# Kernel optimization log

Hardware: AMD Instinct MI355X
Metric: run time of the kernel (lower is better)

The kernel has to match this reference:

```python
import jax, jax.numpy as jnp
import numpy as np

N = 50000          # residues
E = 1000000        # edges
H = 128            # hidden_channels
CUT = 11.5         # cutoff
NR = 6             # num_radial
NS = 3             # num_spherical
NPE = 16           # num_pos_emb

def swish(x):
    return x * jax.nn.sigmoid(x)

def rbf(d):
    # Bessel-style radial basis with smooth cosine cutoff, [E, NR]
    u = jnp.clip(d / CUT, 0.0, 1.0)
    n = jnp.arange(1, NR + 1, dtype=jnp.float32)
    fc = 0.5 * (jnp.cos(jnp.pi * u) + 1.0)
    return jnp.sqrt(2.0 / CUT) * jnp.sin(n * jnp.pi * u[:, None]) / (d[:, None] + 1e-6) * fc[:, None]

def angle_emb(d, ang):
    # d_angle_emb: radial x cos(l*angle) -> [E, NR*NS]
    r = rbf(d)
    l = jnp.arange(NS, dtype=jnp.float32)
    a = jnp.cos(ang[:, None] * l)
    return (r[:, :, None] * a[:, None, :]).reshape(d.shape[0], NR * NS)

def theta_phi_emb(d, theta, phi):
    # d_theta_phi_emb: radial x angular(theta) x angular(phi) -> [E, NR*NS*NS]
    r = rbf(d)
    l = jnp.arange(NS, dtype=jnp.float32)
    ct = jnp.cos(theta[:, None] * l)
    cp = jnp.cos(phi[:, None] * l)
    return jnp.einsum('en,el,em->enlm', r, ct, cp).reshape(d.shape[0], NR * NS * NS)


def setup_inputs():
    key = jax.random.key(0)
    ks = jax.random.split(key, 20)
    f32 = jnp.float32
    pos = jax.random.normal(ks[0], (N, 3), f32) * 8.0
    pos_n = pos + jax.random.normal(ks[1], (N, 3), f32) * 0.8
    pos_c = pos + jax.random.normal(ks[2], (N, 3), f32) * 0.8
    z = jax.random.randint(ks[3], (N,), 0, 26)
    bb_embs = jax.random.normal(ks[4], (N, 6), f32)
    side_chain_embs = jax.random.normal(ks[5], (N, 8), f32)
    esm_embs = jax.random.normal(ks[6], (N, 1280), f32)
    batch = jnp.zeros((N,), jnp.int32)
    edge_index = jax.random.randint(ks[7], (2, E), 0, N)
    def w(k, shape):
        return jax.random.normal(k, shape, f32) * (1.0 / np.sqrt(shape[0]))
    edge_in = NR * NS * NS + 3 * NR * NS + NPE  # 54 + 54 + 16 = 124
    params = dict(
        W_emb=w(ks[8], (26 + 6 + 8, H // 2)), b_emb=jnp.zeros((H // 2,), f32),
        W_esm=w(ks[9], (1280, H // 2)), b_esm=jnp.zeros((H // 2,), f32),
        W_edge=w(ks[10], (edge_in, H)),
        W_msg=w(ks[11], (H, H)),
        W_upd=w(ks[12], (H, H)),
        W_o0=w(ks[13], (H, H)), b_o0=jnp.zeros((H,), f32),
        W_o1=w(ks[14], (H, 32)), b_o1=jnp.zeros((32,), f32),
        W_of=w(ks[15], (32, 1)), b_of=jnp.zeros((1,), f32),
        W_n0=w(ks[16], (H, 32)), b_n0=jnp.zeros((32,), f32),
        W_nf=w(ks[17], (32, 2)), b_nf=jnp.zeros((2,), f32),
    )
    return dict(z=z, pos=pos, pos_n=pos_n, pos_c=pos_c, bb_embs=bb_embs,
                side_chain_embs=side_chain_embs, esm_embs=esm_embs,
                batch=batch, edge_index=edge_index, **params)


def reference(z, pos, pos_n, pos_c, bb_embs, side_chain_embs, esm_embs, batch,
              edge_index, W_emb, b_emb, W_esm, b_esm, W_edge, W_msg, W_upd,
              W_o0, b_o0, W_o1, b_o1, W_of, b_of, W_n0, b_n0, W_nf, b_nf):
    # --- node embedding fusion (level='allatom+esm') ---
    oh = jax.nn.one_hot(z, 26, dtype=jnp.float32)
    x_a = jnp.concatenate([oh, bb_embs, side_chain_embs], axis=1) @ W_emb + b_emb
    x_s = esm_embs @ W_esm + b_esm
    x = jnp.concatenate([x_a, x_s], axis=-1)  # [N, H]

    j, i = edge_index[0], edge_index[1]

    # --- sinusoidal positional embedding of sequence offsets ---
    dpe = (j - i).astype(jnp.float32)
    freq = jnp.exp(jnp.arange(0, NPE, 2, dtype=jnp.float32) * (-np.log(10000.0) / NPE))
    ang = dpe[:, None] * freq
    pe = jnp.concatenate([jnp.cos(ang), jnp.sin(ang)], axis=-1)  # [E, NPE]

    # --- distance / theta / phi (triplet gathers via sequence neighbors) ---
    v_ji = pos[j] - pos[i]
    dist = jnp.linalg.norm(pos[i] - pos[j], axis=1)
    refi0 = (i - 1) % N
    refi1 = (i + 1) % N
    v_r0 = pos[refi0] - pos[i]
    v_r1 = pos[refi1] - pos[i]
    a = jnp.sum(v_ji * v_r0, axis=-1)
    b = jnp.linalg.norm(jnp.cross(v_ji, v_r0), axis=-1)
    theta = jnp.arctan2(b, a)
    p1 = jnp.cross(v_r0, v_r1)
    p2 = jnp.cross(v_r0, v_ji)
    a = jnp.sum(p1 * p2, axis=-1)
    b = jnp.sum(jnp.cross(p1, p2) * v_r0, axis=-1) / (jnp.linalg.norm(v_r0, axis=-1) + 1e-7)
    phi = jnp.arctan2(b, a)
    feature0 = theta_phi_emb(dist, theta, phi)  # [E, 54]

    # --- backbone-frame Euler angles (allatom branch) ---
    o1x = pos_n[i] - pos[i]
    o1z = jnp.cross(o1x, jnp.cross(o1x, pos_c[i] - pos[i]))
    o1zl = jnp.linalg.norm(o1z, axis=1) + 1e-7
    o2x = pos_n[j] - pos[j]
    o2z = jnp.cross(o2x, jnp.cross(o2x, pos_c[j] - pos[j]))
    o2zl = jnp.linalg.norm(o2z, axis=1) + 1e-7
    nvec = jnp.cross(o1z, o2z)
    angle1 = jnp.arctan2(jnp.sum(jnp.cross(o1x, nvec) * o1z, -1) / o1zl, jnp.sum(o1x * nvec, -1))
    angle2 = jnp.arctan2(jnp.linalg.norm(nvec, axis=-1), jnp.sum(o1z * o2z, -1))
    angle3 = jnp.arctan2(jnp.sum(jnp.cross(nvec, o2x) * o2z, -1) / o2zl, jnp.sum(nvec * o2x, -1))
    feature1 = jnp.concatenate([angle_emb(dist, angle1), angle_emb(dist, angle2),
                                angle_emb(dist, angle3)], axis=1)  # [E, 54]

    # --- message passing (gather-compute-scatter stand-in for model_E) ---
    ef = swish(jnp.concatenate([feature0, feature1, pe], axis=-1) @ W_edge)  # [E, H]
    m = swish(x[j] @ W_msg) * ef
    agg = jax.ops.segment_sum(m, i, num_segments=N)
    xe = x + swish(agg @ W_upd)

    # --- output heads (dropout inactive at inference) ---
    xn = jax.nn.relu(x @ W_n0 + b_n0)
    node_out = xn @ W_nf + b_nf                   # [N, 2]
    h = jax.nn.relu(xe @ W_o0 + b_o0)
    h = jax.nn.relu(h @ W_o1 + b_o1)
    out = jax.nn.sigmoid(h @ W_of + b_of)         # [N, 1]
    return out, node_out
```

## Files before the change

kernel.cpp:

```cpp
#include <hip/hip_runtime.h>
#include <math.h>
#include <stdint.h>

#define NRES 50000
#define NEDGE 1000000
#define PI_F 3.14159265358979323846f

typedef __attribute__((ext_vector_type(8))) short short8;
typedef __attribute__((ext_vector_type(4))) float floatx4;
typedef __attribute__((ext_vector_type(2))) short bf16x2;
typedef __attribute__((address_space(1))) bf16x2* gbf16x2p;

struct f3 { float x, y, z; };
__device__ __forceinline__ f3 ld3(const float* __restrict__ p, int i) {
  return {p[3*i+0], p[3*i+1], p[3*i+2]};
}
__device__ __forceinline__ f3 f3sub(f3 a, f3 b){ return {a.x-b.x, a.y-b.y, a.z-b.z}; }
__device__ __forceinline__ f3 f3cross(f3 a, f3 b){
  return {a.y*b.z - a.z*b.y, a.z*b.x - a.x*b.z, a.x*b.y - a.y*b.x};
}
__device__ __forceinline__ float f3dot(f3 a, f3 b){ return a.x*b.x + a.y*b.y + a.z*b.z; }
__device__ __forceinline__ float swish_fast(float v){
  return v * __builtin_amdgcn_rcpf(1.0f + __expf(-v));
}
__device__ __forceinline__ short f2bf(float f){
  unsigned u = __float_as_uint(f);
  unsigned r = (u + 0x7fffu + ((u >> 16) & 1u)) >> 16;
  return (short)r;
}
__device__ __forceinline__ float bf2f(short s){
  return __uint_as_float(((unsigned)(unsigned short)s) << 16);
}
__device__ __forceinline__ float cos_atan2(float y, float x){
  return x * __builtin_amdgcn_rsqf(fmaxf(x*x + y*y, 1e-30f));
}
__device__ __forceinline__ void atom_pk_bf16(short* addr, bf16x2 v){
  __builtin_amdgcn_global_atomic_fadd_v2bf16((gbf16x2p)(uintptr_t)addr, v);
}

__global__ __launch_bounds__(256) void k_wprep(
    const float* __restrict__ We, const float* __restrict__ Wm,
    const float* __restrict__ Ws, const float* __restrict__ Wu,
    const float* __restrict__ Wo0, const float* __restrict__ Wn0,
    const float* __restrict__ Wo1,
    short* __restrict__ Wef, short* __restrict__ Wmf, short* __restrict__ Wsf,
    short* __restrict__ Wuf, short* __restrict__ Wo0f,
    short* __restrict__ Wn0f, short* __restrict__ Wo1f)
{
  int gid = blockIdx.x * 256 + threadIdx.x;
  const float* src; short* dst; int NT, K, N, t;
  if      (gid < 16384)  { t = gid;          src = We;  dst = Wef;  NT = 8; K = 124;  N = 128; }
  else if (gid < 32768)  { t = gid - 16384;  src = Wm;  dst = Wmf;  NT = 8; K = 128;  N = 128; }
  else if (gid < 114688) { t = gid - 32768;  src = Ws;  dst = Wsf;  NT = 4; K = 1280; N = 64;  }
  else if (gid < 131072) { t = gid - 114688; src = Wu;  dst = Wuf;  NT = 8; K = 128;  N = 128; }
  else if (gid < 147456) { t = gid - 131072; src = Wo0; dst = Wo0f; NT = 8; K = 128;  N = 128; }
  else if (gid < 151552) { t = gid - 147456; src = Wn0; dst = Wn0f; NT = 2; K = 128;  N = 32;  }
  else if (gid < 155648) { t = gid - 151552; src = Wo1; dst = Wo1f; NT = 2; K = 128;  N = 32;  }
  else return;
  int j = t & 7, lane = (t >> 3) & 63;
  int rest = t >> 9;
  int nt = rest % NT, kt = rest / NT;
  int k = kt*32 + (lane >> 4)*8 + j, n = nt*16 + (lane & 15);
  dst[t] = f2bf((k < K) ? src[k*N + n] : 0.0f);
}

__global__ __launch_bounds__(256) void k_xa(
    const int* __restrict__ z, const float* __restrict__ bb,
    const float* __restrict__ side, const float* __restrict__ W_emb,
    const float* __restrict__ b_emb, short* __restrict__ xb)
{
  int tid = threadIdx.x;
  int h = tid & 63;
  int n = blockIdx.x * 4 + (tid >> 6);
  if (n >= NRES) return;
  int zz = z[n];
  float acc = W_emb[zz * 64 + h] + b_emb[h];
  #pragma unroll
  for (int k = 0; k < 6; ++k) acc += bb[n*6 + k] * W_emb[(26 + k)*64 + h];
  #pragma unroll
  for (int k = 0; k < 8; ++k) acc += side[n*8 + k] * W_emb[(32 + k)*64 + h];
  xb[(size_t)n * 128 + h] = f2bf(acc);
}

__global__ __launch_bounds__(256) void k_esm(
    const float* __restrict__ esm, const short* __restrict__ Wsf,
    const float* __restrict__ b, short* __restrict__ xb)
{
  const int tid = threadIdx.x;
  const int lane = tid & 63, w = tid >> 6;
  const int quad = lane >> 4, colb = lane & 15;
  const int tile0 = blockIdx.x * 64 + w * 16;

  int arow = tile0 + colb;
  if (arow >= NRES) arow = NRES - 1;
  const float* ap = esm + (size_t)arow * 1280 + quad * 8;

  floatx4 acc[4];
  #pragma unroll
  for (int nt = 0; nt < 4; ++nt) acc[nt] = (floatx4){0.f, 0.f, 0.f, 0.f};

  for (int kt = 0; kt < 40; ++kt) {
    float4 v0 = *(const float4*)(ap + kt*32);
    float4 v1 = *(const float4*)(ap + kt*32 + 4);
    short8 a;
    a[0] = f2bf(v0.x); a[1] = f2bf(v0.y); a[2] = f2bf(v0.z); a[3] = f2bf(v0.w);
    a[4] = f2bf(v1.x); a[5] = f2bf(v1.y); a[6] = f2bf(v1.z); a[7] = f2bf(v1.w);
    #pragma unroll
    for (int nt = 0; nt < 4; ++nt) {
      short8 bf = *(const short8*)&Wsf[(size_t)((kt*4 + nt)*64 + lane)*8];
      acc[nt] = __builtin_amdgcn_mfma_f32_16x16x32_bf16(a, bf, acc[nt], 0, 0, 0);
    }
  }
  #pragma unroll
  for (int nt = 0; nt < 4; ++nt) {
    int ch = nt*16 + colb;
    float bias = b[ch];
    #pragma unroll
    for (int r = 0; r < 4; ++r) {
      int n = tile0 + quad*4 + r;
      if (n < NRES) xb[(size_t)n * 128 + 64 + ch] = f2bf(acc[nt][r] + bias);
    }
  }
}

__global__ __launch_bounds__(256, 4) void k_edge(
    const int* __restrict__ ei, const float* __restrict__ pos,
    const float* __restrict__ posn, const float* __restrict__ posc,
    const short* __restrict__ xb, const short* __restrict__ Wef,
    const short* __restrict__ Wmf, short* __restrict__ aggb)
{
  __shared__ int sJ[64];
  __shared__ int sI[64];
  __shared__ __align__(16) short sF[64][136];
  __shared__ __align__(16) short sXJ[64][136];

  const int tid = threadIdx.x;
  const int e0 = blockIdx.x * 64;

  if (tid < 64) { sJ[tid] = ei[e0 + tid]; sI[tid] = ei[NEDGE + e0 + tid]; }
  __syncthreads();

  if (tid < 64) {
    const int e = tid;
    const int j = sJ[e], i = sI[e];
    f3 pj = ld3(pos, j), pi = ld3(pos, i);
    f3 vji = f3sub(pj, pi);
    float nji2 = f3dot(vji, vji);
    float dist = sqrtf(nji2);
    int r0i = (i == 0) ? (NRES - 1) : (i - 1);
    int r1i = (i == NRES - 1) ? 0 : (i + 1);
    f3 vr0 = f3sub(ld3(pos, r0i), pi);
    f3 vr1 = f3sub(ld3(pos, r1i), pi);
    float nr02 = f3dot(vr0, vr0);

    float ct = f3dot(vji, vr0) * __builtin_amdgcn_rsqf(fmaxf(nji2 * nr02, 1e-30f));
    f3 p1 = f3cross(vr0, vr1);
    f3 p2 = f3cross(vr0, vji);
    float pa = f3dot(p1, p2);
    float pb = f3dot(f3cross(p1, p2), vr0) / (sqrtf(nr02) + 1e-7f);
    float cp = cos_atan2(pb, pa);

    f3 pni = ld3(posn, i), pci = ld3(posc, i);
    f3 o1x = f3sub(pni, pi);
    f3 o1z = f3cross(o1x, f3cross(o1x, f3sub(pci, pi)));
    float no1z2 = f3dot(o1z, o1z);
    float o1zl = sqrtf(no1z2) + 1e-7f;
    f3 pnj = ld3(posn, j), pcj = ld3(posc, j);
    f3 o2x = f3sub(pnj, pj);
    f3 o2z = f3cross(o2x, f3cross(o2x, f3sub(pcj, pj)));
    float no2z2 = f3dot(o2z, o2z);
    float o2zl = sqrtf(no2z2) + 1e-7f;
    f3 nv = f3cross(o1z, o2z);
    float y1 = f3dot(f3cross(o1x, nv), o1z) / o1zl;
    float ca1 = cos_atan2(y1, f3dot(o1x, nv));
    float ca2 = f3dot(o1z, o2z) * __builtin_amdgcn_rsqf(fmaxf(no1z2 * no2z2, 1e-30f));
    float y3 = f3dot(f3cross(nv, o2x), o2z) / o2zl;
    float ca3 = cos_atan2(y3, f3dot(nv, o2x));

    float u = fminf(dist * (1.0f/11.5f), 1.0f);
    float spu, cpu;
    __sincosf(PI_F * u, &spu, &cpu);
    float fc = 0.5f * (cpu + 1.0f);
    float pref = 0.41702882811414954f * __builtin_amdgcn_rcpf(dist + 1e-6f) * fc;
    float rb[6];
    {
      float twoc = 2.0f * cpu;
      float s_nm1 = 0.0f, s_n = spu;
      #pragma unroll
      for (int nn = 0; nn < 6; ++nn) {
        rb[nn] = pref * s_n;
        float s_np1 = twoc * s_n - s_nm1;
        s_nm1 = s_n; s_n = s_np1;
      }
    }

    float ctv[3] = {1.0f, ct, 2.0f*ct*ct - 1.0f};
    float cpv[3] = {1.0f, cp, 2.0f*cp*cp - 1.0f};
    #pragma unroll
    for (int nn = 0; nn < 6; ++nn)
      #pragma unroll
      for (int l = 0; l < 3; ++l)
        #pragma unroll
        for (int m = 0; m < 3; ++m)
          sF[e][nn*9 + l*3 + m] = f2bf(rb[nn] * ctv[l] * cpv[m]);

    float cas[3] = {ca1, ca2, ca3};
    #pragma unroll
    for (int t = 0; t < 3; ++t) {
      float c = cas[t];
      float cav[3] = {1.0f, c, 2.0f*c*c - 1.0f};
      #pragma unroll
      for (int nn = 0; nn < 6; ++nn)
        #pragma unroll
        for (int l = 0; l < 3; ++l)
          sF[e][54 + t*18 + nn*3 + l] = f2bf(rb[nn] * cav[l]);
    }

    const float FRQ[8] = {1.0f, 0.31622776601683794f, 0.1f, 0.03162277660168379f,
                          0.01f, 0.003162277660168379f, 0.001f, 0.0003162277660168379f};
    float dpe = (float)(j - i);
    #pragma unroll
    for (int q = 0; q < 8; ++q) {
      float s, c;
      __sincosf(dpe * FRQ[q], &s, &c);
      sF[e][108 + q] = f2bf(c);
      sF[e][116 + q] = f2bf(s);
    }
    sF[e][124] = 0; sF[e][125] = 0; sF[e][126] = 0; sF[e][127] = 0;
  } else {
    const int t2 = tid - 64;
    for (int it = 0; it < 6; ++it) {
      int idx = it * 192 + t2;
      if (idx < 1024) {
        int row = idx >> 4;
        int c8 = idx & 15;
        *(short8*)&sXJ[row][c8*8] = *(const short8*)&xb[(size_t)sJ[row] * 128 + c8*8];
      }
    }
  }
  __syncthreads();

  const int lane = tid & 63, w = tid >> 6;
  const int quad = lane >> 4, colb = lane & 15;
  const int nb = w * 2;

  short8 bE[4][2], bM[4][2];
  #pragma unroll
  for (int kt = 0; kt < 4; ++kt)
    #pragma unroll
    for (int nt = 0; nt < 2; ++nt) {
      bE[kt][nt] = *(const short8*)&Wef[(size_t)((kt*8 + nb + nt)*64 + lane)*8];
      bM[kt][nt] = *(const short8*)&Wmf[(size_t)((kt*8 + nb + nt)*64 + lane)*8];
    }

  floatx4 accE[4][2], accM[4][2];
  #pragma unroll
  for (int mt = 0; mt < 4; ++mt)
    #pragma unroll
    for (int nt = 0; nt < 2; ++nt) {
      accE[mt][nt] = (floatx4){0.f, 0.f, 0.f, 0.f};
      accM[mt][nt] = (floatx4){0.f, 0.f, 0.f, 0.f};
    }

  #pragma unroll
  for (int kt = 0; kt < 4; ++kt) {
    #pragma unroll
    for (int mt = 0; mt < 4; ++mt) {
      short8 af = *(const short8*)&sF [mt*16 + colb][kt*32 + quad*8];
      short8 ax = *(const short8*)&sXJ[mt*16 + colb][kt*32 + quad*8];
      #pragma unroll
      for (int nt = 0; nt < 2; ++nt) {
        accE[mt][nt] = __builtin_amdgcn_mfma_f32_16x16x32_bf16(af, bE[kt][nt], accE[mt][nt], 0, 0, 0);
        accM[mt][nt] = __builtin_amdgcn_mfma_f32_16x16x32_bf16(ax, bM[kt][nt], accM[mt][nt], 0, 0, 0);
      }
    }
  }
  __syncthreads();

  short (*sM)[136] = sXJ;
  #pragma unroll
  for (int mt = 0; mt < 4; ++mt)
    #pragma unroll
    for (int nt = 0; nt < 2; ++nt) {
      int ch = w*32 + nt*16 + colb;
      #pragma unroll
      for (int r = 0; r < 4; ++r) {
        int e = mt*16 + quad*4 + r;
        sM[e][ch] = f2bf(swish_fast(accM[mt][nt][r]) * swish_fast(accE[mt][nt][r]));
      }
    }
  __syncthreads();

  #pragma unroll
  for (int it = 0; it < 16; ++it) {
    int flat = it * 256 + tid;
    int row = flat >> 6, p = flat & 63;
    bf16x2 v = *(const bf16x2*)&sM[row][p*2];
    atom_pk_bf16(&aggb[(size_t)sI[row] * 128 + p*2], v);
  }
}

__global__ __launch_bounds__(256) void k_upd(
    const short* __restrict__ xb, const short* __restrict__ aggb,
    const short* __restrict__ Wuf, const short* __restrict__ Wo0f,
    const short* __restrict__ Wn0f, const short* __restrict__ Wo1f,
    const float* __restrict__ bn0, const float* __restrict__ Wnf,
    const float* __restrict__ bnf, const float* __restrict__ bo0,
    const float* __restrict__ bo1, const float* __restrict__ Wof,
    const float* __restrict__ bof, float* __restrict__ out0,
    float* __restrict__ out1)
{
  __shared__ __align__(16) short sA[64][136];
  __shared__ __align__(16) short sX[64][136];
  __shared__ float sS[64][33];

  const int tid = threadIdx.x;
  const int lane = tid & 63, w = tid >> 6;
  const int quad = lane >> 4, colb = lane & 15;
  const int n0 = blockIdx.x * 64;

  #pragma unroll
  for (int it = 0; it < 4; ++it) {
    int idx = it * 256 + tid;
    int row = idx >> 4, c8 = idx & 15;
    int n = n0 + row;
    short8 va = (short8)(short)0, vx = (short8)(short)0;
    if (n < NRES) {
      va = *(const short8*)&aggb[(size_t)n * 128 + c8*8];
      vx = *(const short8*)&xb  [(size_t)n * 128 + c8*8];
    }
    *(short8*)&sA[row][c8*8] = va;
    *(short8*)&sX[row][c8*8] = vx;
  }
  __syncthreads();

  {
    floatx4 accN[2];
    accN[0] = (floatx4){0.f,0.f,0.f,0.f}; accN[1] = (floatx4){0.f,0.f,0.f,0.f};
    #pragma unroll
    for (int kt = 0; kt < 4; ++kt) {
      short8 a = *(const short8*)&sX[w*16 + colb][kt*32 + quad*8];
      #pragma unroll
      for (int nt = 0; nt < 2; ++nt) {
        short8 bf = *(const short8*)&Wn0f[(size_t)((kt*2 + nt)*64 + lane)*8];
        accN[nt] = __builtin_amdgcn_mfma_f32_16x16x32_bf16(a, bf, accN[nt], 0, 0, 0);
      }
    }
    #pragma unroll
    for (int nt = 0; nt < 2; ++nt) {
      int col = nt*16 + colb;
      float bias = bn0[col];
      #pragma unroll
      for (int r = 0; r < 4; ++r)
        sS[w*16 + quad*4 + r][col] = fmaxf(accN[nt][r] + bias, 0.0f);
    }
  }
  __syncthreads();
  if (tid < 128) {
    int row = tid >> 1, oc = tid & 1;
    int n = n0 + row;
    if (n < NRES) {
      float a2 = bnf[oc];
      #pragma unroll
      for (int k = 0; k < 32; ++k) a2 += sS[row][k] * Wnf[k*2 + oc];
      out1[(size_t)n * 2 + oc] = a2;
    }
  }

  floatx4 acc1[4][2];
  #pragma unroll
  for (int mt = 0; mt < 4; ++mt) {
    acc1[mt][0] = (floatx4){0.f,0.f,0.f,0.f};
    acc1[mt][1] = (floatx4){0.f,0.f,0.f,0.f};
  }
  #pragma unroll
  for (int kt = 0; kt < 4; ++kt) {
    short8 b0 = *(const short8*)&Wuf[(size_t)((kt*8 + w*2 + 0)*64 + lane)*8];
    short8 b1 = *(const short8*)&Wuf[(size_t)((kt*8 + w*2 + 1)*64 + lane)*8];
    #pragma unroll
    for (int mt = 0; mt < 4; ++mt) {
      short8 a = *(const short8*)&sA[mt*16 + colb][kt*32 + quad*8];
      acc1[mt][0] = __builtin_amdgcn_mfma_f32_16x16x32_bf16(a, b0, acc1[mt][0], 0, 0, 0);
      acc1[mt][1] = __builtin_amdgcn_mfma_f32_16x16x32_bf16(a, b1, acc1[mt][1], 0, 0, 0);
    }
  }
  __syncthreads();
  #pragma unroll
  for (int mt = 0; mt < 4; ++mt)
    #pragma unroll
    for (int nt = 0; nt < 2; ++nt)
      #pragma unroll
      for (int r = 0; r < 4; ++r) {
        int row = mt*16 + quad*4 + r, col = w*32 + nt*16 + colb;
        float xv = bf2f(sX[row][col]);
        sA[row][col] = f2bf(xv + swish_fast(acc1[mt][nt][r]));
      }
  __syncthreads();

  floatx4 acc2[4][2];
  #pragma unroll
  for (int mt = 0; mt < 4; ++mt) {
    acc2[mt][0] = (floatx4){0.f,0.f,0.f,0.f};
    acc2[mt][1] = (floatx4){0.f,0.f,0.f,0.f};
  }
  #pragma unroll
  for (int kt = 0; kt < 4; ++kt) {
    short8 b0 = *(const short8*)&Wo0f[(size_t)((kt*8 + w*2 + 0)*64 + lane)*8];
    short8 b1 = *(const short8*)&Wo0f[(size_t)((kt*8 + w*2 + 1)*64 + lane)*8];
    #pragma unroll
    for (int mt = 0; mt < 4; ++mt) {
      short8 a = *(const short8*)&sA[mt*16 + colb][kt*32 + quad*8];
      acc2[mt][0] = __builtin_amdgcn_mfma_f32_16x16x32_bf16(a, b0, acc2[mt][0], 0, 0, 0);
      acc2[mt][1] = __builtin_amdgcn_mfma_f32_16x16x32_bf16(a, b1, acc2[mt][1], 0, 0, 0);
    }
  }
  __syncthreads();
  #pragma unroll
  for (int mt = 0; mt < 4; ++mt)
    #pragma unroll
    for (int nt = 0; nt < 2; ++nt) {
      int col = w*32 + nt*16 + colb;
      float bias = bo0[col];
      #pragma unroll
      for (int r = 0; r < 4; ++r) {
        int row = mt*16 + quad*4 + r;
        sX[row][col] = f2bf(fmaxf(acc2[mt][nt][r] + bias, 0.0f));
      }
    }
  __syncthreads();

  {
    floatx4 accH[2];
    accH[0] = (floatx4){0.f,0.f,0.f,0.f}; accH[1] = (floatx4){0.f,0.f,0.f,0.f};
    #pragma unroll
    for (int kt = 0; kt < 4; ++kt) {
      short8 a = *(const short8*)&sX[w*16 + colb][kt*32 + quad*8];
      #pragma unroll
      for (int nt = 0; nt < 2; ++nt) {
        short8 bf = *(const short8*)&Wo1f[(size_t)((kt*2 + nt)*64 + lane)*8];
        accH[nt] = __builtin_amdgcn_mfma_f32_16x16x32_bf16(a, bf, accH[nt], 0, 0, 0);
      }
    }
    __syncthreads();
    #pragma unroll
    for (int nt = 0; nt < 2; ++nt) {
      int col = nt*16 + colb;
      float bias = bo1[col];
      #pragma unroll
      for (int r = 0; r < 4; ++r)
        sS[w*16 + quad*4 + r][col] = fmaxf(accH[nt][r] + bias, 0.0f);
    }
  }
  __syncthreads();

  if (tid < 64) {
    int n = n0 + tid;
    if (n < NRES) {
      float a2 = bof[0];
      #pragma unroll
      for (int k = 0; k < 32; ++k) a2 += sS[tid][k] * Wof[k];
      out0[n] = 1.0f / (1.0f + expf(-a2));
    }
  }
}

extern "C" void kernel_launch(void* const* d_in, const int* in_sizes, int n_in,
                              void* d_out, int out_size, void* d_ws, size_t ws_size,
                              hipStream_t stream) {
  (void)in_sizes; (void)n_in; (void)out_size; (void)ws_size;
  const int*   z     = (const int*)  d_in[0];
  const float* pos   = (const float*)d_in[1];
  const float* posn  = (const float*)d_in[2];
  const float* posc  = (const float*)d_in[3];
  const float* bb    = (const float*)d_in[4];
  const float* side  = (const float*)d_in[5];
  const float* esm   = (const float*)d_in[6];
  const int*   ei    = (const int*)  d_in[8];
  const float* W_emb = (const float*)d_in[9];
  const float* b_emb = (const float*)d_in[10];
  const float* W_esm = (const float*)d_in[11];
  const float* b_esm = (const float*)d_in[12];
  const float* W_edge= (const float*)d_in[13];
  const float* W_msg = (const float*)d_in[14];
  const float* W_upd = (const float*)d_in[15];
  const float* W_o0  = (const float*)d_in[16];
  const float* b_o0  = (const float*)d_in[17];
  const float* W_o1  = (const float*)d_in[18];
  const float* b_o1  = (const float*)d_in[19];
  const float* W_of  = (const float*)d_in[20];
  const float* b_of  = (const float*)d_in[21];
  const float* W_n0  = (const float*)d_in[22];
  const float* b_n0  = (const float*)d_in[23];
  const float* W_nf  = (const float*)d_in[24];
  const float* b_nf  = (const float*)d_in[25];

  char* ws = (char*)d_ws;
  short* xb   = (short*)ws;
  short* aggb = (short*)(ws + 12800000);
  short* Wef  = (short*)(ws + 25600000);
  short* Wmf  = (short*)(ws + 25632768);
  short* Wsf  = (short*)(ws + 25665536);
  short* Wuf  = (short*)(ws + 25829376);
  short* Wo0f = (short*)(ws + 25862144);
  short* Wn0f = (short*)(ws + 25894912);
  short* Wo1f = (short*)(ws + 25903104);
  float* out0 = (float*)d_out;
  float* out1 = out0 + NRES;

  hipMemsetAsync(aggb, 0, (size_t)NRES * 128 * sizeof(short), stream);

  k_wprep<<<608, 256, 0, stream>>>(W_edge, W_msg, W_esm, W_upd, W_o0, W_n0, W_o1,
                                   Wef, Wmf, Wsf, Wuf, Wo0f, Wn0f, Wo1f);
  k_xa   <<<12500, 256, 0, stream>>>(z, bb, side, W_emb, b_emb, xb);
  k_esm  <<<782,   256, 0, stream>>>(esm, Wsf, b_esm, xb);
  k_edge <<<15625, 256, 0, stream>>>(ei, pos, posn, posc, xb, Wef, Wmf, aggb);
  k_upd  <<<782,   256, 0, stream>>>(xb, aggb, Wuf, Wo0f, Wn0f, Wo1f,
                                     b_n0, W_nf, b_nf, b_o0, b_o1, W_of, b_of,
                                     out0, out1);
}
```

Baseline: 712.0 us.

## Precompute per-node message transform and sort edges by destination for segmented atomics

Moves the swish(x[j] @ W_msg) projection out of the per-edge kernel into a per-node k_msg kernel, so the edge kernel gathers precomputed messages instead of doing a second GEMM for every edge. Edges are counting-sorted by destination (histogram, scan, scatter) into a permutation, and the edge kernel walks sorted edges, reducing rows with the same destination locally before issuing bf16 atomics. Blocks are remapped across XCDs so contiguous sorted chunks stay together. This adds several small sort kernels and a permuted gather, and it runs only when the workspace is large enough, otherwise falling back to the old path.

```diff
diff --git a/kernel.cpp b/kernel.cpp
--- a/kernel.cpp
+++ b/kernel.cpp
@@ -5,6 +5,7 @@
 #define NRES 50000
 #define NEDGE 1000000
 #define PI_F 3.14159265358979323846f
+#define NSEG 196
 
 typedef __attribute__((ext_vector_type(8))) short short8;
 typedef __attribute__((ext_vector_type(4))) float floatx4;
@@ -36,6 +37,97 @@
 }
 __device__ __forceinline__ void atom_pk_bf16(short* addr, bf16x2 v){
   __builtin_amdgcn_global_atomic_fadd_v2bf16((gbf16x2p)(uintptr_t)addr, v);
+}
+
+__device__ __forceinline__ void edge_features(
+    int e, int j, int i,
+    const float* __restrict__ pos, const float* __restrict__ posn,
+    const float* __restrict__ posc, short (*sF)[136])
+{
+  f3 pj = ld3(pos, j), pi = ld3(pos, i);
+  f3 vji = f3sub(pj, pi);
+  float nji2 = f3dot(vji, vji);
+  float dist = sqrtf(nji2);
+  int r0i = (i == 0) ? (NRES - 1) : (i - 1);
+  int r1i = (i == NRES - 1) ? 0 : (i + 1);
+  f3 vr0 = f3sub(ld3(pos, r0i), pi);
+  f3 vr1 = f3sub(ld3(pos, r1i), pi);
+  float nr02 = f3dot(vr0, vr0);
+
+  float ct = f3dot(vji, vr0) * __builtin_amdgcn_rsqf(fmaxf(nji2 * nr02, 1e-30f));
+  f3 p1 = f3cross(vr0, vr1);
+  f3 p2 = f3cross(vr0, vji);
+  float pa = f3dot(p1, p2);
+  float pb = f3dot(f3cross(p1, p2), vr0) / (sqrtf(nr02) + 1e-7f);
+  float cp = cos_atan2(pb, pa);
+
+  f3 pni = ld3(posn, i), pci = ld3(posc, i);
+  f3 o1x = f3sub(pni, pi);
+  f3 o1z = f3cross(o1x, f3cross(o1x, f3sub(pci, pi)));
+  float no1z2 = f3dot(o1z, o1z);
+  float o1zl = sqrtf(no1z2) + 1e-7f;
+  f3 pnj = ld3(posn, j), pcj = ld3(posc, j);
+  f3 o2x = f3sub(pnj, pj);
+  f3 o2z = f3cross(o2x, f3cross(o2x, f3sub(pcj, pj)));
+  float no2z2 = f3dot(o2z, o2z);
+  float o2zl = sqrtf(no2z2) + 1e-7f;
+  f3 nv = f3cross(o1z, o2z);
+  float y1 = f3dot(f3cross(o1x, nv), o1z) / o1zl;
+  float ca1 = cos_atan2(y1, f3dot(o1x, nv));
+  float ca2 = f3dot(o1z, o2z) * __builtin_amdgcn_rsqf(fmaxf(no1z2 * no2z2, 1e-30f));
+  float y3 = f3dot(f3cross(nv, o2x), o2z) / o2zl;
+  float ca3 = cos_atan2(y3, f3dot(nv, o2x));
+
+  float u = fminf(dist * (1.0f/11.5f), 1.0f);
+  float spu, cpu;
+  __sincosf(PI_F * u, &spu, &cpu);
+  float fc = 0.5f * (cpu + 1.0f);
+  float pref = 0.41702882811414954f * __builtin_amdgcn_rcpf(dist + 1e-6f) * fc;
+  float rb[6];
+  {
+    float twoc = 2.0f * cpu;
+    float s_nm1 = 0.0f, s_n = spu;
+    #pragma unroll
+    for (int nn = 0; nn < 6; ++nn) {
+      rb[nn] = pref * s_n;
+      float s_np1 = twoc * s_n - s_nm1;
+      s_nm1 = s_n; s_n = s_np1;
+    }
+  }
+
+  float ctv[3] = {1.0f, ct, 2.0f*ct*ct - 1.0f};
+  float cpv[3] = {1.0f, cp, 2.0f*cp*cp - 1.0f};
+  #pragma unroll
+  for (int nn = 0; nn < 6; ++nn)
+    #pragma unroll
+    for (int l = 0; l < 3; ++l)
+      #pragma unroll
+      for (int m = 0; m < 3; ++m)
+        sF[e][nn*9 + l*3 + m] = f2bf(rb[nn] * ctv[l] * cpv[m]);
+
+  float cas[3] = {ca1, ca2, ca3};
+  #pragma unroll
+  for (int t = 0; t < 3; ++t) {
+    float c = cas[t];
+    float cav[3] = {1.0f, c, 2.0f*c*c - 1.0f};
+    #pragma unroll
+    for (int nn = 0; nn < 6; ++nn)
+      #pragma unroll
+      for (int l = 0; l < 3; ++l)
+        sF[e][54 + t*18 + nn*3 + l] = f2bf(rb[nn] * cav[l]);
+  }
+
+  const float FRQ[8] = {1.0f, 0.31622776601683794f, 0.1f, 0.03162277660168379f,
+                        0.01f, 0.003162277660168379f, 0.001f, 0.0003162277660168379f};
+  float dpe = (float)(j - i);
+  #pragma unroll
+  for (int q = 0; q < 8; ++q) {
+    float s, c;
+    __sincosf(dpe * FRQ[q], &s, &c);
+    sF[e][108 + q] = f2bf(c);
+    sF[e][116 + q] = f2bf(s);
+  }
+  sF[e][124] = 0; sF[e][125] = 0; sF[e][126] = 0; sF[e][127] = 0;
 }
 
 __global__ __launch_bounds__(256) void k_wprep(
@@ -64,6 +156,68 @@
   dst[t] = f2bf((k < K) ? src[k*N + n] : 0.0f);
 }
 
+__global__ __launch_bounds__(256) void k_hist(
+    const int* __restrict__ ei, int* __restrict__ bins)
+{
+  int e = blockIdx.x * 256 + threadIdx.x;
+  if (e < NEDGE) atomicAdd(&bins[ei[NEDGE + e]], 1);
+}
+
+__global__ __launch_bounds__(256) void k_scan1(
+    int* __restrict__ bins, int* __restrict__ bsum)
+{
+  __shared__ int s[256];
+  const int t = threadIdx.x, b = blockIdx.x;
+  const int idx = b * 256 + t;
+  int v = (idx < NRES) ? bins[idx] : 0;
+  s[t] = v;
+  __syncthreads();
+  #pragma unroll
+  for (int d = 1; d < 256; d <<= 1) {
+    int add = (t >= d) ? s[t - d] : 0;
+    __syncthreads();
+    if (t >= d) s[t] += add;
+    __syncthreads();
+  }
+  if (idx < NRES) bins[idx] = s[t] - v;
+  if (t == 255) bsum[b] = s[255];
+}
+
+__global__ __launch_bounds__(256) void k_scan2(int* __restrict__ bsum)
+{
+  __shared__ int s[256];
+  const int t = threadIdx.x;
+  int v = (t < NSEG) ? bsum[t] : 0;
+  s[t] = v;
+  __syncthreads();
+  #pragma unroll
+  for (int d = 1; d < 256; d <<= 1) {
+    int add = (t >= d) ? s[t - d] : 0;
+    __syncthreads();
+    if (t >= d) s[t] += add;
+    __syncthreads();
+  }
+  if (t < NSEG) bsum[t] = s[t] - v;
+}
+
+__global__ __launch_bounds__(256) void k_scan3(
+    int* __restrict__ bins, const int* __restrict__ bsum)
+{
+  int idx = blockIdx.x * 256 + threadIdx.x;
+  if (idx < NRES) bins[idx] += bsum[blockIdx.x];
+}
+
+__global__ __launch_bounds__(256) void k_scatter(
+    const int* __restrict__ ei, int* __restrict__ bins, int* __restrict__ perm)
+{
+  int e = blockIdx.x * 256 + threadIdx.x;
+  if (e < NEDGE) {
+    int i = ei[NEDGE + e];
+    int slot = atomicAdd(&bins[i], 1);
+    if (slot >= 0 && slot < NEDGE) perm[slot] = e;
+  }
+}
+
 __global__ __launch_bounds__(256) void k_xa(
     const int* __restrict__ z, const float* __restrict__ bb,
     const float* __restrict__ side, const float* __restrict__ W_emb,
@@ -123,7 +277,172 @@
   }
 }
 
-__global__ __launch_bounds__(256, 4) void k_edge(
+__global__ __launch_bounds__(256) void k_msg(
+    const short* __restrict__ xb, const short* __restrict__ Wmf,
+    short* __restrict__ xmb)
+{
+  __shared__ __align__(16) short sX[64][136];
+  __shared__ __align__(16) short sO[64][136];
+  const int tid = threadIdx.x;
+  const int lane = tid & 63, w = tid >> 6;
+  const int quad = lane >> 4, colb = lane & 15;
+  const int n0 = blockIdx.x * 64;
+
+  #pragma unroll
+  for (int it = 0; it < 4; ++it) {
+    int idx = it * 256 + tid;
+    int row = idx >> 4, c8 = idx & 15;
+    int n = n0 + row;
+    short8 v = (short8)(short)0;
+    if (n < NRES) v = *(const short8*)&xb[(size_t)n * 128 + c8*8];
+    *(short8*)&sX[row][c8*8] = v;
+  }
+  __syncthreads();
+
+  floatx4 acc[4][2];
+  #pragma unroll
+  for (int mt = 0; mt < 4; ++mt) {
+    acc[mt][0] = (floatx4){0.f,0.f,0.f,0.f};
+    acc[mt][1] = (floatx4){0.f,0.f,0.f,0.f};
+  }
+  #pragma unroll
+  for (int kt = 0; kt < 4; ++kt) {
+    short8 b0 = *(const short8*)&Wmf[(size_t)((kt*8 + w*2 + 0)*64 + lane)*8];
+    short8 b1 = *(const short8*)&Wmf[(size_t)((kt*8 + w*2 + 1)*64 + lane)*8];
+    #pragma unroll
+    for (int mt = 0; mt < 4; ++mt) {
+      short8 a = *(const short8*)&sX[mt*16 + colb][kt*32 + quad*8];
+      acc[mt][0] = __builtin_amdgcn_mfma_f32_16x16x32_bf16(a, b0, acc[mt][0], 0, 0, 0);
+      acc[mt][1] = __builtin_amdgcn_mfma_f32_16x16x32_bf16(a, b1, acc[mt][1], 0, 0, 0);
+    }
+  }
+  #pragma unroll
+  for (int mt = 0; mt < 4; ++mt)
+    #pragma unroll
+    for (int nt = 0; nt < 2; ++nt)
+      #pragma unroll
+      for (int r = 0; r < 4; ++r)
+        sO[mt*16 + quad*4 + r][w*32 + nt*16 + colb] = f2bf(swish_fast(acc[mt][nt][r]));
+  __syncthreads();
+  #pragma unroll
+  for (int it = 0; it < 4; ++it) {
+    int idx = it * 256 + tid;
+    int row = idx >> 4, c8 = idx & 15;
+    int n = n0 + row;
+    if (n < NRES) *(short8*)&xmb[(size_t)n * 128 + c8*8] = *(short8*)&sO[row][c8*8];
+  }
+}
+
+__global__ __launch_bounds__(256, 4) void k_edge_s(
+    const int* __restrict__ perm, const int* __restrict__ ei,
+    const float* __restrict__ pos,
+    const float* __restrict__ posn, const float* __restrict__ posc,
+    const short* __restrict__ xmb, const short* __restrict__ Wef,
+    short* __restrict__ aggb)
+{
+  __shared__ int sJ[64];
+  __shared__ int sI[64];
+  __shared__ __align__(16) short sF[64][136];
+  __shared__ __align__(16) short sXJ[64][136];
+
+  const int tid = threadIdx.x;
+  const int orig = blockIdx.x;
+  const int xcd = orig & 7, sub = orig >> 3;
+  const int wg = (xcd == 0 ? 0 : 1954 + (xcd - 1) * 1953) + sub;
+  const int e0 = wg * 64;
+
+  if (tid < 64) {
+    int ep = perm[e0 + tid];
+    ep = (ep < 0) ? 0 : ((ep >= NEDGE) ? NEDGE - 1 : ep);
+    int jj = ei[ep], ii = ei[NEDGE + ep];
+    sJ[tid] = (jj < 0) ? 0 : ((jj >= NRES) ? NRES - 1 : jj);
+    sI[tid] = (ii < 0) ? 0 : ((ii >= NRES) ? NRES - 1 : ii);
+  }
+  __syncthreads();
+
+  if (tid < 64) {
+    edge_features(tid, sJ[tid], sI[tid], pos, posn, posc, sF);
+  } else {
+    const int t2 = tid - 64;
+    for (int it = 0; it < 6; ++it) {
+      int idx = it * 192 + t2;
+      if (idx < 1024) {
+        int row = idx >> 4;
+        int c8 = idx & 15;
+        *(short8*)&sXJ[row][c8*8] = *(const short8*)&xmb[(size_t)sJ[row] * 128 + c8*8];
+      }
+    }
+  }
+  __syncthreads();
+
+  const int lane = tid & 63, w = tid >> 6;
+  const int quad = lane >> 4, colb = lane & 15;
+  const int nb = w * 2;
+
+  short8 bE[4][2];
+  #pragma unroll
+  for (int kt = 0; kt < 4; ++kt)
+    #pragma unroll
+    for (int nt = 0; nt < 2; ++nt)
+      bE[kt][nt] = *(const short8*)&Wef[(size_t)((kt*8 + nb + nt)*64 + lane)*8];
+
+  floatx4 accE[4][2];
+  #pragma unroll
+  for (int mt = 0; mt < 4; ++mt) {
+    accE[mt][0] = (floatx4){0.f, 0.f, 0.f, 0.f};
+    accE[mt][1] = (floatx4){0.f, 0.f, 0.f, 0.f};
+  }
+
+  #pragma unroll
+  for (int kt = 0; kt < 4; ++kt) {
+    #pragma unroll
+    for (int mt = 0; mt < 4; ++mt) {
+      short8 af = *(const short8*)&sF[mt*16 + colb][kt*32 + quad*8];
+      #pragma unroll
+      for (int nt = 0; nt < 2; ++nt)
+        accE[mt][nt] = __builtin_amdgcn_mfma_f32_16x16x32_bf16(af, bE[kt][nt], accE[mt][nt], 0, 0, 0);
+    }
+  }
+  __syncthreads();
+
+  short (*sM)[136] = sF;
+  #pragma unroll
+  for (int mt = 0; mt < 4; ++mt)
+    #pragma unroll
+    for (int nt = 0; nt < 2; ++nt) {
+      int ch = w*32 + nt*16 + colb;
+      #pragma unroll
+      for (int r = 0; r < 4; ++r) {
+        int e = mt*16 + quad*4 + r;
+        float mv = bf2f(sXJ[e][ch]) * swish_fast(accE[mt][nt][r]);
+        sM[e][ch] = f2bf(mv);
+      }
+    }
+  __syncthreads();
+
+  {
+    const int p = tid & 63;
+    const int g = tid >> 6;
+    float ax = 0.f, ay = 0.f;
+    int cur = sI[g * 16];
+    #pragma unroll
+    for (int rr = 0; rr < 16; ++rr) {
+      int row = g * 16 + rr;
+      int ii = sI[row];
+      if (ii != cur) {
+        bf16x2 v; v[0] = f2bf(ax); v[1] = f2bf(ay);
+        atom_pk_bf16(&aggb[(size_t)cur * 128 + p*2], v);
+        ax = 0.f; ay = 0.f; cur = ii;
+      }
+      bf16x2 mv = *(const bf16x2*)&sM[row][p*2];
+      ax += bf2f(mv[0]); ay += bf2f(mv[1]);
+    }
+    bf16x2 v; v[0] = f2bf(ax); v[1] = f2bf(ay);
+    atom_pk_bf16(&aggb[(size_t)cur * 128 + p*2], v);
+  }
+}
+
+__global__ __launch_bounds__(256, 4) void k_edge_b(
     const int* __restrict__ ei, const float* __restrict__ pos,
     const float* __restrict__ posn, const float* __restrict__ posc,
     const short* __restrict__ xb, const short* __restrict__ Wef,
@@ -141,92 +460,7 @@
   __syncthreads();
 
   if (tid < 64) {
-    const int e = tid;
-    const int j = sJ[e], i = sI[e];
-    f3 pj = ld3(pos, j), pi = ld3(pos, i);
-    f3 vji = f3sub(pj, pi);
-    float nji2 = f3dot(vji, vji);
-    float dist = sqrtf(nji2);
-    int r0i = (i == 0) ? (NRES - 1) : (i - 1);
-    int r1i = (i == NRES - 1) ? 0 : (i + 1);
-    f3 vr0 = f3sub(ld3(pos, r0i), pi);
-    f3 vr1 = f3sub(ld3(pos, r1i), pi);
-    float nr02 = f3dot(vr0, vr0);
-
-    float ct = f3dot(vji, vr0) * __builtin_amdgcn_rsqf(fmaxf(nji2 * nr02, 1e-30f));
-    f3 p1 = f3cross(vr0, vr1);
-    f3 p2 = f3cross(vr0, vji);
-    float pa = f3dot(p1, p2);
-    float pb = f3dot(f3cross(p1, p2), vr0) / (sqrtf(nr02) + 1e-7f);
-    float cp = cos_atan2(pb, pa);
-
-    f3 pni = ld3(posn, i), pci = ld3(posc, i);
-    f3 o1x = f3sub(pni, pi);
-    f3 o1z = f3cross(o1x, f3cross(o1x, f3sub(pci, pi)));
-    float no1z2 = f3dot(o1z, o1z);
-    float o1zl = sqrtf(no1z2) + 1e-7f;
-    f3 pnj = ld3(posn, j), pcj = ld3(posc, j);
-    f3 o2x = f3sub(pnj, pj);
-    f3 o2z = f3cross(o2x, f3cross(o2x, f3sub(pcj, pj)));
-    float no2z2 = f3dot(o2z, o2z);
-    float o2zl = sqrtf(no2z2) + 1e-7f;
-    f3 nv = f3cross(o1z, o2z);
-    float y1 = f3dot(f3cross(o1x, nv), o1z) / o1zl;
-    float ca1 = cos_atan2(y1, f3dot(o1x, nv));
-    float ca2 = f3dot(o1z, o2z) * __builtin_amdgcn_rsqf(fmaxf(no1z2 * no2z2, 1e-30f));
-    float y3 = f3dot(f3cross(nv, o2x), o2z) / o2zl;
-    float ca3 = cos_atan2(y3, f3dot(nv, o2x));
-
-    float u = fminf(dist * (1.0f/11.5f), 1.0f);
-    float spu, cpu;
-    __sincosf(PI_F * u, &spu, &cpu);
-    float fc = 0.5f * (cpu + 1.0f);
-    float pref = 0.41702882811414954f * __builtin_amdgcn_rcpf(dist + 1e-6f) * fc;
-    float rb[6];
-    {
-      float twoc = 2.0f * cpu;
-      float s_nm1 = 0.0f, s_n = spu;
-      #pragma unroll
-      for (int nn = 0; nn < 6; ++nn) {
-        rb[nn] = pref * s_n;
-        float s_np1 = twoc * s_n - s_nm1;
-        s_nm1 = s_n; s_n = s_np1;
-      }
-    }
-
-    float ctv[3] = {1.0f, ct, 2.0f*ct*ct - 1.0f};
-    float cpv[3] = {1.0f, cp, 2.0f*cp*cp - 1.0f};
-    #pragma unroll
-    for (int nn = 0; nn < 6; ++nn)
-      #pragma unroll
-      for (int l = 0; l < 3; ++l)
-        #pragma unroll
-        for (int m = 0; m < 3; ++m)
-          sF[e][nn*9 + l*3 + m] = f2bf(rb[nn] * ctv[l] * cpv[m]);
-
-    float cas[3] = {ca1, ca2, ca3};
-    #pragma unroll
-    for (int t = 0; t < 3; ++t) {
-      float c = cas[t];
-      float cav[3] = {1.0f, c, 2.0f*c*c - 1.0f};
-      #pragma unroll
-      for (int nn = 0; nn < 6; ++nn)
-        #pragma unroll
-        for (int l = 0; l < 3; ++l)
-          sF[e][54 + t*18 + nn*3 + l] = f2bf(rb[nn] * cav[l]);
-    }
-
-    const float FRQ[8] = {1.0f, 0.31622776601683794f, 0.1f, 0.03162277660168379f,
-                          0.01f, 0.003162277660168379f, 0.001f, 0.0003162277660168379f};
-    float dpe = (float)(j - i);
-    #pragma unroll
-    for (int q = 0; q < 8; ++q) {
-      float s, c;
-      __sincosf(dpe * FRQ[q], &s, &c);
-      sF[e][108 + q] = f2bf(c);
-      sF[e][116 + q] = f2bf(s);
-    }
-    sF[e][124] = 0; sF[e][125] = 0; sF[e][126] = 0; sF[e][127] = 0;
+    edge_features(tid, sJ[tid], sI[tid], pos, posn, posc, sF);
   } else {
     const int t2 = tid - 64;
     for (int it = 0; it < 6; ++it) {
@@ -467,7 +701,7 @@
 extern "C" void kernel_launch(void* const* d_in, const int* in_sizes, int n_in,
                               void* d_out, int out_size, void* d_ws, size_t ws_size,
                               hipStream_t stream) {
-  (void)in_sizes; (void)n_in; (void)out_size; (void)ws_size;
+  (void)in_sizes; (void)n_in; (void)out_size;
   const int*   z     = (const int*)  d_in[0];
   const float* pos   = (const float*)d_in[1];
   const float* posn  = (const float*)d_in[2];
@@ -494,27 +728,64 @@
   const float* W_nf  = (const float*)d_in[24];
   const float* b_nf  = (const float*)d_in[25];
 
-  char* ws = (char*)d_ws;
-  short* xb   = (short*)ws;
-  short* aggb = (short*)(ws + 12800000);
-  short* Wef  = (short*)(ws + 25600000);
-  short* Wmf  = (short*)(ws + 25632768);
-  short* Wsf  = (short*)(ws + 25665536);
-  short* Wuf  = (short*)(ws + 25829376);
-  short* Wo0f = (short*)(ws + 25862144);
-  short* Wn0f = (short*)(ws + 25894912);
-  short* Wo1f = (short*)(ws + 25903104);
   float* out0 = (float*)d_out;
   float* out1 = out0 + NRES;
-
-  hipMemsetAsync(aggb, 0, (size_t)NRES * 128 * sizeof(short), stream);
-
-  k_wprep<<<608, 256, 0, stream>>>(W_edge, W_msg, W_esm, W_upd, W_o0, W_n0, W_o1,
-                                   Wef, Wmf, Wsf, Wuf, Wo0f, Wn0f, Wo1f);
-  k_xa   <<<12500, 256, 0, stream>>>(z, bb, side, W_emb, b_emb, xb);
-  k_esm  <<<782,   256, 0, stream>>>(esm, Wsf, b_esm, xb);
-  k_edge <<<15625, 256, 0, stream>>>(ei, pos, posn, posc, xb, Wef, Wmf, aggb);
-  k_upd  <<<782,   256, 0, stream>>>(xb, aggb, Wuf, Wo0f, Wn0f, Wo1f,
-                                     b_n0, W_nf, b_nf, b_o0, b_o1, W_of, b_of,
-                                     out0, out1);
-}
+  char* ws = (char*)d_ws;
+
+  const bool full = (ws_size >= (size_t)42912096);
+
+  if (full) {
+    short* xb   = (short*)ws;
+    short* aggb = (short*)(ws + 12800000);
+    short* xmb  = (short*)(ws + 25600000);
+    short* Wef  = (short*)(ws + 38400000);
+    short* Wmf  = (short*)(ws + 38432768);
+    short* Wsf  = (short*)(ws + 38465536);
+    short* Wuf  = (short*)(ws + 38629376);
+    short* Wo0f = (short*)(ws + 38662144);
+    short* Wn0f = (short*)(ws + 38694912);
+    short* Wo1f = (short*)(ws + 38703104);
+    int*   bins = (int*)  (ws + 38711296);
+    int*   bsum = (int*)  (ws + 38911296);
+    int*   perm = (int*)  (ws + 38912096);
+
+    hipMemsetAsync(aggb, 0, (size_t)NRES * 128 * sizeof(short), stream);
+    hipMemsetAsync(bins, 0, (size_t)NRES * sizeof(int), stream);
+
+    k_wprep  <<<608, 256, 0, stream>>>(W_edge, W_msg, W_esm, W_upd, W_o0, W_n0, W_o1,
+                                       Wef, Wmf, Wsf, Wuf, Wo0f, Wn0f, Wo1f);
+    k_hist   <<<3907, 256, 0, stream>>>(ei, bins);
+    k_scan1  <<<NSEG, 256, 0, stream>>>(bins, bsum);
+    k_scan2  <<<1,    256, 0, stream>>>(bsum);
+    k_scan3  <<<NSEG, 256, 0, stream>>>(bins, bsum);
+    k_scatter<<<3907, 256, 0, stream>>>(ei, bins, perm);
+    k_xa     <<<12500, 256, 0, stream>>>(z, bb, side, W_emb, b_emb, xb);
+    k_esm    <<<782,   256, 0, stream>>>(esm, Wsf, b_esm, xb);
+    k_msg    <<<782,   256, 0, stream>>>(xb, Wmf, xmb);
+    k_edge_s <<<15625, 256, 0, stream>>>(perm, ei, pos, posn, posc, xmb, Wef, aggb);
+    k_upd    <<<782,   256, 0, stream>>>(xb, aggb, Wuf, Wo0f, Wn0f, Wo1f,
+                                         b_n0, W_nf, b_nf, b_o0, b_o1, W_of, b_of,
+                                         out0, out1);
+  } else {
+    short* xb   = (short*)ws;
+    short* aggb = (short*)(ws + 12800000);
+    short* Wef  = (short*)(ws + 25600000);
+    short* Wmf  = (short*)(ws + 25632768);
+    short* Wsf  = (short*)(ws + 25665536);
+    short* Wuf  = (short*)(ws + 25829376);
+    short* Wo0f = (short*)(ws + 25862144);
+    short* Wn0f = (short*)(ws + 25894912);
+    short* Wo1f = (short*)(ws + 25903104);
+
+    hipMemsetAsync(aggb, 0, (size_t)NRES * 128 * sizeof(short), stream);
+
+    k_wprep <<<608, 256, 0, stream>>>(W_edge, W_msg, W_esm, W_upd, W_o0, W_n0, W_o1,
+                                      Wef, Wmf, Wsf, Wuf, Wo0f, Wn0f, Wo1f);
+    k_xa    <<<12500, 256, 0, stream>>>(z, bb, side, W_emb, b_emb, xb);
+    k_esm   <<<782,   256, 0, stream>>>(esm, Wsf, b_esm, xb);
+    k_edge_b<<<15625, 256, 0, stream>>>(ei, pos, posn, posc, xb, Wef, Wmf, aggb);
+    k_upd   <<<782,   256, 0, stream>>>(xb, aggb, Wuf, Wo0f, Wn0f, Wo1f,
+                                        b_n0, W_nf, b_nf, b_o0, b_o1, W_of, b_of,
+                                        out0, out1);
+  }
+}
```

After: 728.5 us. 2.3% more time.
